# Optimization experiments

Measured on AMD Instinct MI355X. Metric: run time of the kernel, lower is better.

Reference implementation:

```python
import jax, jax.numpy as jnp
import numpy as np

N_NODES = 100000
D_GRAPH = 512    # graph_embedding_dim
D_ROUTE = 1024   # routes_embedding_dim
N_ROUTES = 16384
ROUTE_LEN = 32
N_BLOCKS = 3


def setup_inputs() -> dict:
    key = jax.random.key(0)
    ks = jax.random.split(key, 2 + 2 * N_BLOCKS)
    graph_embedding = jax.random.normal(ks[0], (N_NODES, D_GRAPH), dtype=jnp.float32)
    locations_idx = jax.random.randint(ks[1], (N_ROUTES, ROUTE_LEN), 0, N_NODES, dtype=jnp.int64)
    # Linear block chain: first block D_GRAPH->D_ROUTE, rest D_ROUTE->D_ROUTE, ReLU each
    dims = [D_GRAPH] + [D_ROUTE] * N_BLOCKS
    inp = {"graph_embedding": graph_embedding, "locations_idx": locations_idx}
    for i in range(N_BLOCKS):
        fan_in = dims[i]
        scale = 1.0 / np.sqrt(fan_in)
        inp[f"W{i}"] = jax.random.uniform(ks[2 + 2 * i], (fan_in, dims[i + 1]), jnp.float32, -scale, scale)
        inp[f"b{i}"] = jax.random.uniform(ks[3 + 2 * i], (dims[i + 1],), jnp.float32, -scale, scale)
    return inp


def reference(graph_embedding, locations_idx, W0, b0, W1, b1, W2, b2):
    # per-route gather: [R, L, D] then max over route positions -> [R, D]
    gathered = graph_embedding[locations_idx]          # [n_routes, route_len, d_graph]
    routes_emb = jnp.max(gathered, axis=1)             # [n_routes, d_graph]
    # linear block chain (Linear + ReLU per block)
    x = jax.nn.relu(routes_emb @ W0 + b0)
    x = jax.nn.relu(x @ W1 + b1)
    x = jax.nn.relu(x @ W2 + b2)
    return x
```

## Files before the change

kernel.cpp:

```cpp
#include <hip/hip_runtime.h>
#include <hip/hip_bf16.h>
#include <cstdint>


typedef __attribute__((ext_vector_type(8))) short          bf16x8;
typedef __attribute__((ext_vector_type(8))) unsigned short u16x8;
typedef __attribute__((ext_vector_type(4))) float          f32x4;

__device__ __forceinline__ unsigned short f2b_rne(float f) {
    union { float f; uint32_t i; } x; x.f = f;
    uint32_t lsb = (x.i >> 16) & 1u;
    return (unsigned short)((x.i + 0x7fffu + lsb) >> 16);
}

__global__ void transpose_f32_bf16(const float* __restrict__ W,
                                   unsigned short* __restrict__ Wt,
                                   int K, int N)
{
    __shared__ float tile[32][33];
    const int n0 = blockIdx.x * 32;
    const int k0 = blockIdx.y * 32;
    const int tx = threadIdx.x & 31;
    const int ty = threadIdx.x >> 5;
#pragma unroll
    for (int i = 0; i < 32; i += 8)
        tile[ty + i][tx] = W[(size_t)(k0 + ty + i) * N + (n0 + tx)];
    __syncthreads();
#pragma unroll
    for (int i = 0; i < 32; i += 8)
        Wt[(size_t)(n0 + ty + i) * K + (k0 + tx)] = f2b_rne(tile[tx][ty + i]);
}

__global__ void gather_max_kernel(const float* __restrict__ graph,
                                  const int* __restrict__ idx32,
                                  unsigned short* __restrict__ routes)
{
    bool is64 = true;
#pragma unroll
    for (int k = 0; k < 64; k++) is64 &= (idx32[2 * k + 1] == 0);
    const int stride = is64 ? 64 : 32;
    const int step   = is64 ? 2  : 1;

    const int wave  = threadIdx.x >> 6;
    const int lane  = threadIdx.x & 63;
    const int route = blockIdx.x * 4 + wave;
    const int col   = lane * 8;

    float m[8];
#pragma unroll
    for (int j = 0; j < 8; j++) m[j] = -INFINITY;

    const int* ip = idx32 + (size_t)route * stride;
#pragma unroll 4
    for (int l = 0; l < 32; l++) {
        const int node = ip[l * step];
        const float4* p = reinterpret_cast<const float4*>(graph + (size_t)node * 512 + col);
        float4 v0 = p[0];
        float4 v1 = p[1];
        m[0] = fmaxf(m[0], v0.x); m[1] = fmaxf(m[1], v0.y);
        m[2] = fmaxf(m[2], v0.z); m[3] = fmaxf(m[3], v0.w);
        m[4] = fmaxf(m[4], v1.x); m[5] = fmaxf(m[5], v1.y);
        m[6] = fmaxf(m[6], v1.z); m[7] = fmaxf(m[7], v1.w);
    }
    u16x8 o;
#pragma unroll
    for (int j = 0; j < 8; j++) o[j] = f2b_rne(m[j]);
    *reinterpret_cast<u16x8*>(routes + (size_t)route * 512 + col) = o;
}

#define BM 128
#define BN 128
#define BK 32
#define KPAD 8

template <typename OutT>
__global__ __launch_bounds__(256)
void gemm_bt_relu(const unsigned short* __restrict__ A,
                  const unsigned short* __restrict__ Bt,
                  const float* __restrict__ bias,
                  OutT* __restrict__ C,
                  int M, int N, int K)
{
    __shared__ unsigned short As[BM][BK + KPAD];
    __shared__ unsigned short Bs[BN][BK + KPAD];

    const int tid  = threadIdx.x;
    const int wave = tid >> 6;
    const int lane = tid & 63;
    const int quad = lane >> 4;
    const int l16  = lane & 15;
    const int wm   = (wave >> 1) * 64;
    const int wn   = (wave & 1) * 64;

    const int bm = blockIdx.y * BM;
    const int bn = blockIdx.x * BN;

    const int sm = tid >> 1;
    const int sk = (tid & 1) * 16;

    const unsigned short* Aptr = A  + (size_t)(bm + sm) * K + sk;
    const unsigned short* Bptr = Bt + (size_t)(bn + sm) * K + sk;

    f32x4 acc[4][4] = {};

    for (int k0 = 0; k0 < K; k0 += BK) {
        const uint4* ap = reinterpret_cast<const uint4*>(Aptr + k0);
        const uint4* bp = reinterpret_cast<const uint4*>(Bptr + k0);
        uint4 a0 = ap[0], a1 = ap[1];
        uint4 b0 = bp[0], b1 = bp[1];
        *reinterpret_cast<uint4*>(&As[sm][sk])     = a0;
        *reinterpret_cast<uint4*>(&As[sm][sk + 8]) = a1;
        *reinterpret_cast<uint4*>(&Bs[sm][sk])     = b0;
        *reinterpret_cast<uint4*>(&Bs[sm][sk + 8]) = b1;
        __syncthreads();

        bf16x8 a[4], b[4];
#pragma unroll
        for (int i = 0; i < 4; i++)
            a[i] = *reinterpret_cast<const bf16x8*>(&As[wm + i * 16 + l16][quad * 8]);
#pragma unroll
        for (int i = 0; i < 4; i++)
            b[i] = *reinterpret_cast<const bf16x8*>(&Bs[wn + i * 16 + l16][quad * 8]);

#pragma unroll
        for (int mi = 0; mi < 4; mi++)
#pragma unroll
            for (int ni = 0; ni < 4; ni++)
                acc[mi][ni] = __builtin_amdgcn_mfma_f32_16x16x32_bf16(
                    a[mi], b[ni], acc[mi][ni], 0, 0, 0);
        __syncthreads();
    }

#pragma unroll
    for (int ni = 0; ni < 4; ni++) {
        const int n  = bn + wn + ni * 16 + l16;
        const float bv = bias[n];
#pragma unroll
        for (int mi = 0; mi < 4; mi++) {
            const int mbase = bm + wm + mi * 16 + quad * 4;
#pragma unroll
            for (int r = 0; r < 4; r++) {
                float v = acc[mi][ni][r] + bv;
                v = fmaxf(v, 0.0f);
                if constexpr (sizeof(OutT) == 2)
                    C[(size_t)(mbase + r) * N + n] = (OutT)f2b_rne(v);
                else
                    C[(size_t)(mbase + r) * N + n] = (OutT)v;
            }
        }
    }
}

extern "C" void kernel_launch(void* const* d_in, const int* in_sizes, int n_in,
                              void* d_out, int out_size, void* d_ws, size_t ws_size,
                              hipStream_t stream)
{
    constexpr int N_ROUTES = 16384;
    constexpr int D_GRAPH  = 512;
    constexpr int D_ROUTE  = 1024;

    const float* graph = (const float*)d_in[0];
    const int*   idx   = (const int*)d_in[1];
    const float* W0    = (const float*)d_in[2];
    const float* b0    = (const float*)d_in[3];
    const float* W1    = (const float*)d_in[4];
    const float* b1    = (const float*)d_in[5];
    const float* W2    = (const float*)d_in[6];
    const float* b2    = (const float*)d_in[7];
    float*       out   = (float*)d_out;

    char* w = (char*)d_ws;
    unsigned short* Wt0    = (unsigned short*)w; w += (size_t)D_ROUTE * D_GRAPH * 2;
    unsigned short* Wt1    = (unsigned short*)w; w += (size_t)D_ROUTE * D_ROUTE * 2;
    unsigned short* Wt2    = (unsigned short*)w; w += (size_t)D_ROUTE * D_ROUTE * 2;
    unsigned short* routes = (unsigned short*)w; w += (size_t)N_ROUTES * D_GRAPH * 2;
    unsigned short* x1     = (unsigned short*)w; w += (size_t)N_ROUTES * D_ROUTE * 2;
    unsigned short* x2     = (unsigned short*)w; w += (size_t)N_ROUTES * D_ROUTE * 2;

    transpose_f32_bf16<<<dim3(D_ROUTE / 32, D_GRAPH / 32), 256, 0, stream>>>(W0, Wt0, D_GRAPH, D_ROUTE);
    transpose_f32_bf16<<<dim3(D_ROUTE / 32, D_ROUTE / 32), 256, 0, stream>>>(W1, Wt1, D_ROUTE, D_ROUTE);
    transpose_f32_bf16<<<dim3(D_ROUTE / 32, D_ROUTE / 32), 256, 0, stream>>>(W2, Wt2, D_ROUTE, D_ROUTE);

    gather_max_kernel<<<N_ROUTES / 4, 256, 0, stream>>>(graph, idx, routes);

    gemm_bt_relu<unsigned short><<<dim3(D_ROUTE / BN, N_ROUTES / BM), 256, 0, stream>>>(
        routes, Wt0, b0, x1, N_ROUTES, D_ROUTE, D_GRAPH);
    gemm_bt_relu<unsigned short><<<dim3(D_ROUTE / BN, N_ROUTES / BM), 256, 0, stream>>>(
        x1, Wt1, b1, x2, N_ROUTES, D_ROUTE, D_ROUTE);
    gemm_bt_relu<float><<<dim3(D_ROUTE / BN, N_ROUTES / BM), 256, 0, stream>>>(
        x2, Wt2, b2, out, N_ROUTES, D_ROUTE, D_ROUTE);
}
```

Before: 590.9 us.

## Use direct global-to-LDS loads with XOR swizzle in GEMM; two routes per wave in gather

The GEMM tile loads now go straight from global memory into LDS through global_load_lds, skipping the register round trip. The padded LDS rows are replaced by an XOR-swizzled layout so the bf16x8 fragment reads avoid bank conflicts without padding. The gather kernel now has each wave process two routes, with half as many blocks, so more independent loads are in flight per wave. The swizzle has to match between the async store addresses and the fragment reads. The loop is still single-buffered, so loads and MFMA work do not overlap.

```diff
diff --git a/kernel.cpp b/kernel.cpp
--- a/kernel.cpp
+++ b/kernel.cpp
@@ -11,6 +11,12 @@
     union { float f; uint32_t i; } x; x.f = f;
     uint32_t lsb = (x.i >> 16) & 1u;
     return (unsigned short)((x.i + 0x7fffu + lsb) >> 16);
+}
+
+__device__ __forceinline__ void async_copy16(const void* gptr, void* lptr) {
+    __builtin_amdgcn_global_load_lds(
+        (const __attribute__((address_space(1))) unsigned int*)gptr,
+        (__attribute__((address_space(3))) unsigned int*)lptr, 16, 0, 0);
 }
 
 __global__ void transpose_f32_bf16(const float* __restrict__ W,
@@ -43,35 +49,42 @@
 
     const int wave  = threadIdx.x >> 6;
     const int lane  = threadIdx.x & 63;
-    const int route = blockIdx.x * 4 + wave;
+    const int route = (blockIdx.x * 4 + wave) * 2;
     const int col   = lane * 8;
 
-    float m[8];
-#pragma unroll
-    for (int j = 0; j < 8; j++) m[j] = -INFINITY;
-
-    const int* ip = idx32 + (size_t)route * stride;
+    float m0[8], m1[8];
+#pragma unroll
+    for (int j = 0; j < 8; j++) { m0[j] = -INFINITY; m1[j] = -INFINITY; }
+
+    const int* ip0 = idx32 + (size_t)route * stride;
+    const int* ip1 = ip0 + stride;
 #pragma unroll 4
     for (int l = 0; l < 32; l++) {
-        const int node = ip[l * step];
-        const float4* p = reinterpret_cast<const float4*>(graph + (size_t)node * 512 + col);
-        float4 v0 = p[0];
-        float4 v1 = p[1];
-        m[0] = fmaxf(m[0], v0.x); m[1] = fmaxf(m[1], v0.y);
-        m[2] = fmaxf(m[2], v0.z); m[3] = fmaxf(m[3], v0.w);
-        m[4] = fmaxf(m[4], v1.x); m[5] = fmaxf(m[5], v1.y);
-        m[6] = fmaxf(m[6], v1.z); m[7] = fmaxf(m[7], v1.w);
+        const int n0 = ip0[l * step];
+        const int n1 = ip1[l * step];
+        const float4* p0 = reinterpret_cast<const float4*>(graph + (size_t)n0 * 512 + col);
+        const float4* p1 = reinterpret_cast<const float4*>(graph + (size_t)n1 * 512 + col);
+        float4 a0 = p0[0], a1 = p0[1];
+        float4 b0 = p1[0], b1 = p1[1];
+        m0[0] = fmaxf(m0[0], a0.x); m0[1] = fmaxf(m0[1], a0.y);
+        m0[2] = fmaxf(m0[2], a0.z); m0[3] = fmaxf(m0[3], a0.w);
+        m0[4] = fmaxf(m0[4], a1.x); m0[5] = fmaxf(m0[5], a1.y);
+        m0[6] = fmaxf(m0[6], a1.z); m0[7] = fmaxf(m0[7], a1.w);
+        m1[0] = fmaxf(m1[0], b0.x); m1[1] = fmaxf(m1[1], b0.y);
+        m1[2] = fmaxf(m1[2], b0.z); m1[3] = fmaxf(m1[3], b0.w);
+        m1[4] = fmaxf(m1[4], b1.x); m1[5] = fmaxf(m1[5], b1.y);
+        m1[6] = fmaxf(m1[6], b1.z); m1[7] = fmaxf(m1[7], b1.w);
     }
-    u16x8 o;
-#pragma unroll
-    for (int j = 0; j < 8; j++) o[j] = f2b_rne(m[j]);
-    *reinterpret_cast<u16x8*>(routes + (size_t)route * 512 + col) = o;
+    u16x8 o0, o1;
+#pragma unroll
+    for (int j = 0; j < 8; j++) { o0[j] = f2b_rne(m0[j]); o1[j] = f2b_rne(m1[j]); }
+    *reinterpret_cast<u16x8*>(routes + (size_t)route * 512 + col)       = o0;
+    *reinterpret_cast<u16x8*>(routes + (size_t)(route + 1) * 512 + col) = o1;
 }
 
 #define BM 128
 #define BN 128
 #define BK 32
-#define KPAD 8
 
 template <typename OutT>
 __global__ __launch_bounds__(256)
@@ -81,8 +94,8 @@
                   OutT* __restrict__ C,
                   int M, int N, int K)
 {
-    __shared__ unsigned short As[BM][BK + KPAD];
-    __shared__ unsigned short Bs[BN][BK + KPAD];
+    __shared__ unsigned short As[BM * BK];
+    __shared__ unsigned short Bs[BN * BK];
 
     const int tid  = threadIdx.x;
     const int wave = tid >> 6;
@@ -95,32 +108,42 @@
     const int bm = blockIdx.y * BM;
     const int bn = blockIdx.x * BN;
 
-    const int sm = tid >> 1;
-    const int sk = (tid & 1) * 16;
-
-    const unsigned short* Aptr = A  + (size_t)(bm + sm) * K + sk;
-    const unsigned short* Bptr = Bt + (size_t)(bn + sm) * K + sk;
+    const int s0 = wave * 64 + lane;
+    const int s1 = s0 + 256;
+    const int r0 = s0 >> 2, c0 = (s0 & 3) ^ ((r0 >> 1) & 3);
+    const int r1 = s1 >> 2, c1 = (s1 & 3) ^ ((r1 >> 1) & 3);
+
+    const unsigned short* a0g = A  + (size_t)(bm + r0) * K + c0 * 8;
+    const unsigned short* a1g = A  + (size_t)(bm + r1) * K + c1 * 8;
+    const unsigned short* b0g = Bt + (size_t)(bn + r0) * K + c0 * 8;
+    const unsigned short* b1g = Bt + (size_t)(bn + r1) * K + c1 * 8;
+    unsigned short* a0l = As + s0 * 8;
+    unsigned short* a1l = As + s1 * 8;
+    unsigned short* b0l = Bs + s0 * 8;
+    unsigned short* b1l = Bs + s1 * 8;
 
     f32x4 acc[4][4] = {};
 
     for (int k0 = 0; k0 < K; k0 += BK) {
-        const uint4* ap = reinterpret_cast<const uint4*>(Aptr + k0);
-        const uint4* bp = reinterpret_cast<const uint4*>(Bptr + k0);
-        uint4 a0 = ap[0], a1 = ap[1];
-        uint4 b0 = bp[0], b1 = bp[1];
-        *reinterpret_cast<uint4*>(&As[sm][sk])     = a0;
-        *reinterpret_cast<uint4*>(&As[sm][sk + 8]) = a1;
-        *reinterpret_cast<uint4*>(&Bs[sm][sk])     = b0;
-        *reinterpret_cast<uint4*>(&Bs[sm][sk + 8]) = b1;
+        async_copy16(a0g + k0, a0l);
+        async_copy16(a1g + k0, a1l);
+        async_copy16(b0g + k0, b0l);
+        async_copy16(b1g + k0, b1l);
         __syncthreads();
 
         bf16x8 a[4], b[4];
 #pragma unroll
-        for (int i = 0; i < 4; i++)
-            a[i] = *reinterpret_cast<const bf16x8*>(&As[wm + i * 16 + l16][quad * 8]);
-#pragma unroll
-        for (int i = 0; i < 4; i++)
-            b[i] = *reinterpret_cast<const bf16x8*>(&Bs[wn + i * 16 + l16][quad * 8]);
+        for (int i = 0; i < 4; i++) {
+            const int row = wm + i * 16 + l16;
+            const int cp  = quad ^ ((row >> 1) & 3);
+            a[i] = *reinterpret_cast<const bf16x8*>(As + row * BK + cp * 8);
+        }
+#pragma unroll
+        for (int i = 0; i < 4; i++) {
+            const int row = wn + i * 16 + l16;
+            const int cp  = quad ^ ((row >> 1) & 3);
+            b[i] = *reinterpret_cast<const bf16x8*>(Bs + row * BK + cp * 8);
+        }
 
 #pragma unroll
         for (int mi = 0; mi < 4; mi++)
@@ -181,7 +204,7 @@
     transpose_f32_bf16<<<dim3(D_ROUTE / 32, D_ROUTE / 32), 256, 0, stream>>>(W1, Wt1, D_ROUTE, D_ROUTE);
     transpose_f32_bf16<<<dim3(D_ROUTE / 32, D_ROUTE / 32), 256, 0, stream>>>(W2, Wt2, D_ROUTE, D_ROUTE);
 
-    gather_max_kernel<<<N_ROUTES / 4, 256, 0, stream>>>(graph, idx, routes);
+    gather_max_kernel<<<N_ROUTES / 8, 256, 0, stream>>>(graph, idx, routes);
 
     gemm_bt_relu<unsigned short><<<dim3(D_ROUTE / BN, N_ROUTES / BM), 256, 0, stream>>>(
         routes, Wt0, b0, x1, N_ROUTES, D_ROUTE, D_GRAPH);
```

New measurement: 570.4 us. 1.04x faster.
